# Performance work log

Hardware: AMD Instinct MI355X
Metric: run time of the kernel (lower is better)

The kernel has to match this reference:

```python
import jax, jax.numpy as jnp
import numpy as np

B, N1, N2, D, R = 4, 128, 128, 256, 4


def setup_inputs() -> dict:
    key = jax.random.key(0)
    ks = jax.random.split(key, 8)
    s = 0.02  # small init scale for weights
    return {
        "features1": jax.random.normal(ks[0], (B, N1, D), jnp.float32),
        "features2": jax.random.normal(ks[1], (B, N2, D), jnp.float32),
        # relation nets stacked over R: Linear(2D->D), Linear(D->D//2), Linear(D//2->1)
        "W1": jax.random.normal(ks[2], (R, 2 * D, D), jnp.float32) * s,
        "b1": jnp.zeros((R, D), jnp.float32),
        "W2": jax.random.normal(ks[3], (R, D, D // 2), jnp.float32) * s,
        "b2": jnp.zeros((R, D // 2), jnp.float32),
        "w3": jax.random.normal(ks[4], (R, D // 2), jnp.float32) * s,
        "b3": jnp.zeros((R,), jnp.float32),
        # aggregator: Linear(D*R -> 2D), Linear(2D -> D)
        "Wa1": jax.random.normal(ks[5], (D * R, 2 * D), jnp.float32) * s,
        "ba1": jnp.zeros((2 * D,), jnp.float32),
        "Wa2": jax.random.normal(ks[6], (2 * D, D), jnp.float32) * s,
        "ba2": jnp.zeros((D,), jnp.float32),
    }


def reference(features1, features2, W1, b1, W2, b2, w3, b3, Wa1, ba1, Wa2, ba2):
    b, n1, d = features1.shape
    n2 = features2.shape[1]
    r = W1.shape[0]
    # concat([f1_i, f2_j]) @ W1 == f1_i @ W1[:d] + f2_j @ W1[d:]
    W1a, W1b = W1[:, :d, :], W1[:, d:, :]
    h1 = jnp.einsum('bid,rde->brie', features1, W1a)          # [B,R,N1,D]
    h2 = jnp.einsum('bjd,rde->brje', features2, W1b)          # [B,R,N2,D]
    h = jax.nn.relu(h1[:, :, :, None, :] + h2[:, :, None, :, :]
                    + b1[None, :, None, None, :])             # [B,R,N1,N2,D]
    g = jax.nn.relu(jnp.einsum('brijd,rde->brije', h, W2)
                    + b2[None, :, None, None, :])             # [B,R,N1,N2,D//2]
    scores = jnp.einsum('brije,re->brij', g, w3) + b3[None, :, None, None]
    w = jax.nn.softmax(scores, axis=-1)                       # softmax over j (N2)
    rel = jnp.einsum('brij,bjd->brid', w, features2)          # [B,R,N1,D]
    # torch cat over relations along feature dim -> relation index outermost
    all_rel = rel.transpose(0, 2, 1, 3).reshape(b, n1, r * d)  # [B,N1,R*D]
    out = jax.nn.relu(all_rel @ Wa1 + ba1) @ Wa2 + ba2         # [B,N1,D]
    return out
```

## Files before the change

kernel.cpp:

```cpp
#include <hip/hip_runtime.h>


typedef _Float16 f16x8 __attribute__((ext_vector_type(8)));
typedef float f32x16 __attribute__((ext_vector_type(16)));

static __device__ __forceinline__ ushort to_h(float f) {
  _Float16 h = (_Float16)f;
  return __builtin_bit_cast(ushort, h);
}
static __device__ __forceinline__ uint pack2(float a, float b) {
  return (uint)to_h(a) | ((uint)to_h(b) << 16);
}
static __device__ __forceinline__ uint pk_add(uint a, uint b) {
  uint r;
  asm("v_pk_add_f16 %0, %1, %2" : "=v"(r) : "v"(a), "v"(b));
  return r;
}
static __device__ __forceinline__ uint pk_relu(uint a) {
  uint r;
  asm("v_pk_max_f16 %0, %1, %2" : "=v"(r) : "v"(a), "v"(0u));
  return r;
}

__global__ __launch_bounds__(256) void k_prep(
    const float* __restrict__ f1, const float* __restrict__ f2,
    const float* __restrict__ W1, const float* __restrict__ W2,
    const float* __restrict__ Wa1, const float* __restrict__ Wa2,
    uint* __restrict__ f1hp, uint* __restrict__ f2hp,
    ushort* __restrict__ W1swz, ushort* __restrict__ W2swz,
    ushort* __restrict__ f2swz, ushort* __restrict__ Wa1swz,
    ushort* __restrict__ Wa2swz)
{
  int blk = blockIdx.x, t = threadIdx.x;
  if (blk < 128) {
    int u = blk * 256 + t;
    float4 a = *(const float4*)&f1[u * 4];
    float4 b = *(const float4*)&f2[u * 4];
    *(uint2*)&f1hp[u * 2] = make_uint2(pack2(a.x, a.y), pack2(a.z, a.w));
    *(uint2*)&f2hp[u * 2] = make_uint2(pack2(b.x, b.y), pack2(b.z, b.w));
    return;
  }
  if (blk < 256) {
    int unit = blk - 128;
    int r = unit >> 5, half = (unit >> 4) & 1, ks = unit & 15;
    int l = t & 63, ctq = t >> 6;
    #pragma unroll
    for (int ci = 0; ci < 2; ++ci) {
      int ct = ctq + ci * 4;
      int e = ct * 32 + (l & 31);
      ushort us[8];
      #pragma unroll
      for (int j = 0; j < 8; ++j) {
        int d = ks * 16 + ((l >> 5) * 4) + (j & 3) + ((j >> 2) * 8);
        us[j] = to_h(W1[(size_t)(r * 512 + half * 256 + d) * 256 + e]);
      }
      uint4 pk;
      pk.x = (uint)us[0] | ((uint)us[1] << 16);
      pk.y = (uint)us[2] | ((uint)us[3] << 16);
      pk.z = (uint)us[4] | ((uint)us[5] << 16);
      pk.w = (uint)us[6] | ((uint)us[7] << 16);
      *(uint4*)&W1swz[(size_t)((((r * 2 + half) * 16 + ks) * 8 + ct) * 64 + l) * 8] = pk;
    }
    return;
  }
  if (blk < 272) {
    int sub = blk - 256;
    int r = sub >> 2, ks0 = (sub & 3) * 4;
    int ct = t >> 6, l = t & 63;
    #pragma unroll
    for (int ko = 0; ko < 4; ++ko) {
      int ks = ks0 + ko;
      ushort us[8];
      #pragma unroll
      for (int j = 0; j < 8; ++j) {
        int d = ks * 16 + ((j >> 2) * 8) + ((l >> 5) * 4) + (j & 3);
        int e = ct * 32 + (l & 31);
        us[j] = to_h(W2[(r * 256 + d) * 128 + e]);
      }
      uint4 pk;
      pk.x = (uint)us[0] | ((uint)us[1] << 16);
      pk.y = (uint)us[2] | ((uint)us[3] << 16);
      pk.z = (uint)us[4] | ((uint)us[5] << 16);
      pk.w = (uint)us[6] | ((uint)us[7] << 16);
      *(uint4*)&W2swz[(((r * 16 + ks) * 4 + ct) * 64 + l) * 8] = pk;
    }
    return;
  }
  if (blk < 288) {
    int sub = blk - 272;
    int w = t >> 6, l = t & 63;
    #pragma unroll
    for (int ko = 0; ko < 4; ++ko) {
      int u = sub * 16 + w * 4 + ko;
      int b = u >> 6, ks = (u >> 3) & 7, ctg = u & 7;
      ushort us[8];
      #pragma unroll
      for (int j = 0; j < 8; ++j) {
        int k = ks * 16 + ((l >> 5) * 4) + (j & 3) + ((j >> 2) * 8);
        int n = ctg * 32 + (l & 31);
        us[j] = to_h(f2[((size_t)b * 128 + k) * 256 + n]);
      }
      uint4 pk;
      pk.x = (uint)us[0] | ((uint)us[1] << 16);
      pk.y = (uint)us[2] | ((uint)us[3] << 16);
      pk.z = (uint)us[4] | ((uint)us[5] << 16);
      pk.w = (uint)us[6] | ((uint)us[7] << 16);
      *(uint4*)&f2swz[(((b * 8 + ks) * 8 + ctg) * 64 + l) * 8] = pk;
    }
    return;
  }
  if (blk < 304) {
    int sub = blk - 288;
    #pragma unroll
    for (int ko = 0; ko < 16; ++ko) {
      int id = sub * 4096 + ko * 256 + t;
      int ks = id >> 10, ct = (id >> 6) & 15, l = id & 63;
      ushort us[8];
      #pragma unroll
      for (int j = 0; j < 8; ++j) {
        int d = ks * 16 + ((l >> 5) * 4) + (j & 3) + ((j >> 2) * 8);
        int e = ct * 32 + (l & 31);
        us[j] = to_h(Wa1[(size_t)d * 512 + e]);
      }
      uint4 pk;
      pk.x = (uint)us[0] | ((uint)us[1] << 16);
      pk.y = (uint)us[2] | ((uint)us[3] << 16);
      pk.z = (uint)us[4] | ((uint)us[5] << 16);
      pk.w = (uint)us[6] | ((uint)us[7] << 16);
      *(uint4*)&Wa1swz[(size_t)id * 8] = pk;
    }
    return;
  }
  {
    int sub = blk - 304;
    #pragma unroll
    for (int ko = 0; ko < 4; ++ko) {
      int id = sub * 1024 + ko * 256 + t;
      int ks = id >> 9, ct = (id >> 6) & 7, l = id & 63;
      ushort us[8];
      #pragma unroll
      for (int j = 0; j < 8; ++j) {
        int d = ks * 16 + ((l >> 5) * 4) + (j & 3) + ((j >> 2) * 8);
        int e = ct * 32 + (l & 31);
        us[j] = to_h(Wa2[(size_t)d * 256 + e]);
      }
      uint4 pk;
      pk.x = (uint)us[0] | ((uint)us[1] << 16);
      pk.y = (uint)us[2] | ((uint)us[3] << 16);
      pk.z = (uint)us[4] | ((uint)us[5] << 16);
      pk.w = (uint)us[6] | ((uint)us[7] << 16);
      *(uint4*)&Wa2swz[(size_t)id * 8] = pk;
    }
    return;
  }
}

__global__ __launch_bounds__(256) void k_proj_mfma(
    const uint* __restrict__ f1hp, const uint* __restrict__ f2hp,
    const ushort* __restrict__ W1swz, const float* __restrict__ b1,
    ushort* __restrict__ h1p, ushort* __restrict__ h2)
{
  int bid = blockIdx.x;
  int it = bid & 3;
  int half = (bid >> 2) & 1;
  int r = (bid >> 3) & 3;
  int b = bid >> 5;
  int t = threadIdx.x, w = t >> 6, l = t & 63;
  __shared__ uint Au[32][132];

  const uint* src = (half ? f2hp : f1hp) + (size_t)b * 16384 + it * 32 * 128;
  #pragma unroll
  for (int q = 0; q < 4; ++q) {
    int lin = q * 256 + t;
    int row = lin >> 5, c4 = (lin & 31) * 4;
    *(uint4*)&Au[row][c4] = *(const uint4*)&src[row * 128 + c4];
  }
  __syncthreads();

  int m31 = l & 31, hi = l >> 5, hi2 = hi * 2;
  f32x16 acc0, acc1;
  #pragma unroll
  for (int e = 0; e < 16; ++e) { acc0[e] = 0.f; acc1[e] = 0.f; }

  const ushort* bb = W1swz + (size_t)(r * 2 + half) * 65536;
  for (int ks = 0; ks < 16; ++ks) {
    int u0 = ks * 8 + hi2;
    uint2 xa = *(const uint2*)&Au[m31][u0];
    uint2 xb = *(const uint2*)&Au[m31][u0 + 4];
    uint4 a4 = make_uint4(xa.x, xa.y, xb.x, xb.y);
    f16x8 af = __builtin_bit_cast(f16x8, a4);
    uint4 br0 = *(const uint4*)&bb[((ks * 8 + w * 2 + 0) * 64 + l) * 8];
    uint4 br1 = *(const uint4*)&bb[((ks * 8 + w * 2 + 1) * 64 + l) * 8];
    f16x8 bf0 = __builtin_bit_cast(f16x8, br0);
    f16x8 bf1 = __builtin_bit_cast(f16x8, br1);
    acc0 = __builtin_amdgcn_mfma_f32_32x32x16_f16(af, bf0, acc0, 0, 0, 0);
    acc1 = __builtin_amdgcn_mfma_f32_32x32x16_f16(af, bf1, acc1, 0, 0, 0);
  }

  ushort* ho = (half ? h2 : h1p) + ((size_t)((b * 4 + r) * 128 + it * 32)) * 256;
  #pragma unroll
  for (int ctl = 0; ctl < 2; ++ctl) {
    int e = (w * 2 + ctl) * 32 + m31;
    float bv = half ? 0.f : b1[r * 256 + e];
    #pragma unroll
    for (int g = 0; g < 16; ++g) {
      int row = (g & 3) + 8 * (g >> 2) + 4 * hi;
      ho[row * 256 + e] = to_h((ctl ? acc1[g] : acc0[g]) + bv);
    }
  }
}

__global__ __launch_bounds__(256, 4) void k_scores_mfma(
    const ushort* __restrict__ h1p, const ushort* __restrict__ h2,
    const ushort* __restrict__ W2swz, const float* __restrict__ b2,
    const float* __restrict__ w3, const float* __restrict__ b3,
    float* __restrict__ scores)
{
  int bid = blockIdx.x;
  int jt = bid & 7;
  int it = (bid >> 3) & 15;
  int r  = (bid >> 7) & 3;
  int b  = bid >> 9;
  int t = threadIdx.x, w = t >> 6, l = t & 63;
  __shared__ uint h1u[8][132];
  __shared__ uint h2u[16][132];
  __shared__ float xch[4][2][2][16];

  const uint* h1g = (const uint*)h1p + ((size_t)((b * 4 + r) * 128 + it * 8)) * 128;
  const uint* h2g = (const uint*)h2  + ((size_t)((b * 4 + r) * 128 + jt * 16)) * 128;
  {
    int row = t >> 5, c4 = (t & 31) * 4;
    *(uint4*)&h1u[row][c4] = *(const uint4*)&h1g[row * 128 + c4];
    *(uint4*)&h2u[row][c4] = *(const uint4*)&h2g[row * 128 + c4];
    *(uint4*)&h2u[row + 8][c4] = *(const uint4*)&h2g[(row + 8) * 128 + c4];
  }

  f32x16 acc[2][2];
  #pragma unroll
  for (int i = 0; i < 2; ++i)
    #pragma unroll
    for (int c = 0; c < 2; ++c)
      #pragma unroll
      for (int e = 0; e < 16; ++e) acc[i][c][e] = 0.f;

  int rtp = w & 1, ctp = w >> 1;
  int hi2 = (l >> 5) * 2;
  int m31 = l & 31;
  int jrow = m31 & 15;
  int irow0 = (rtp * 2 + 0) * 2 + (m31 >> 4);
  int irow1 = (rtp * 2 + 1) * 2 + (m31 >> 4);
  const ushort* bptr = W2swz + r * (16 * 4 * 64 * 8);

  __syncthreads();

  const uint* h1r0 = &h1u[irow0][0];
  const uint* h1r1 = &h1u[irow1][0];
  const uint* h2r  = &h2u[jrow][0];
  for (int ks = 0; ks < 16; ++ks) {
    int u0 = ks * 8 + hi2;
    uint2 ya  = *(const uint2*)&h2r[u0];
    uint2 yb  = *(const uint2*)&h2r[u0 + 4];
    uint2 xa0 = *(const uint2*)&h1r0[u0];
    uint2 xb0 = *(const uint2*)&h1r0[u0 + 4];
    uint2 xa1 = *(const uint2*)&h1r1[u0];
    uint2 xb1 = *(const uint2*)&h1r1[u0 + 4];
    uint4 pk0, pk1;
    pk0.x = pk_relu(pk_add(xa0.x, ya.x));
    pk0.y = pk_relu(pk_add(xa0.y, ya.y));
    pk0.z = pk_relu(pk_add(xb0.x, yb.x));
    pk0.w = pk_relu(pk_add(xb0.y, yb.y));
    pk1.x = pk_relu(pk_add(xa1.x, ya.x));
    pk1.y = pk_relu(pk_add(xa1.y, ya.y));
    pk1.z = pk_relu(pk_add(xb1.x, yb.x));
    pk1.w = pk_relu(pk_add(xb1.y, yb.y));
    f16x8 af0 = __builtin_bit_cast(f16x8, pk0);
    f16x8 af1 = __builtin_bit_cast(f16x8, pk1);
    uint4 braw0 = *(const uint4*)&bptr[((ks * 4 + ctp * 2 + 0) * 64 + l) * 8];
    uint4 braw1 = *(const uint4*)&bptr[((ks * 4 + ctp * 2 + 1) * 64 + l) * 8];
    f16x8 bf0 = __builtin_bit_cast(f16x8, braw0);
    f16x8 bf1 = __builtin_bit_cast(f16x8, braw1);
    acc[0][0] = __builtin_amdgcn_mfma_f32_32x32x16_f16(af0, bf0, acc[0][0], 0, 0, 0);
    acc[0][1] = __builtin_amdgcn_mfma_f32_32x32x16_f16(af0, bf1, acc[0][1], 0, 0, 0);
    acc[1][0] = __builtin_amdgcn_mfma_f32_32x32x16_f16(af1, bf0, acc[1][0], 0, 0, 0);
    acc[1][1] = __builtin_amdgcn_mfma_f32_32x32x16_f16(af1, bf1, acc[1][1], 0, 0, 0);
  }

  float sp[2][16];
  #pragma unroll
  for (int i = 0; i < 2; ++i)
    #pragma unroll
    for (int g = 0; g < 16; ++g) sp[i][g] = 0.f;
  #pragma unroll
  for (int ctl = 0; ctl < 2; ++ctl) {
    int e = (ctp * 2 + ctl) * 32 + m31;
    float w3v = w3[r * 128 + e];
    float b2v = b2[r * 128 + e];
    #pragma unroll
    for (int i = 0; i < 2; ++i)
      #pragma unroll
      for (int g = 0; g < 16; ++g)
        sp[i][g] = fmaf(w3v, fmaxf(acc[i][ctl][g] + b2v, 0.f), sp[i][g]);
  }
  #pragma unroll
  for (int off = 16; off >= 1; off >>= 1)
    #pragma unroll
    for (int i = 0; i < 2; ++i)
      #pragma unroll
      for (int g = 0; g < 16; ++g)
        sp[i][g] += __shfl_xor(sp[i][g], off, 64);
  int hi = l >> 5;
  if (m31 == 0) {
    #pragma unroll
    for (int i = 0; i < 2; ++i)
      #pragma unroll
      for (int g = 0; g < 16; ++g)
        xch[w][i][hi][g] = sp[i][g];
  }
  __syncthreads();
  if (w < 2 && m31 == 0) {
    float b3v = b3[r];
    float* sc_base = scores + (((b * 4 + r) * 128 + it * 8) * 128) + jt * 16;
    #pragma unroll
    for (int i = 0; i < 2; ++i)
      #pragma unroll
      for (int g = 0; g < 16; ++g) {
        float s = xch[w][i][hi][g] + xch[w + 2][i][hi][g] + b3v;
        int p = (w * 2 + i) * 32 + (g & 3) + 8 * (g >> 2) + hi * 4;
        sc_base[(p >> 4) * 128 + (p & 15)] = s;
      }
  }
}

__global__ __launch_bounds__(64, 1) void k_softrel_mfma(
    const float* __restrict__ scores, const ushort* __restrict__ f2swz,
    ushort* __restrict__ all_rel_h)
{
  int bid = blockIdx.x;
  int rowq = bid & 3;
  int nh = (bid >> 2) & 1;
  int r  = (bid >> 3) & 3;
  int b  = bid >> 5;
  int l = threadIdx.x;
  int row = rowq * 32 + (l & 31);
  const float* srow = scores + ((size_t)(b * 4 + r) * 128 + row) * 128;

  float p[128];
  #pragma unroll
  for (int q = 0; q < 32; ++q) {
    float4 v = *(const float4*)&srow[q * 4];
    p[q * 4 + 0] = v.x; p[q * 4 + 1] = v.y;
    p[q * 4 + 2] = v.z; p[q * 4 + 3] = v.w;
  }
  float m = p[0];
  #pragma unroll
  for (int j = 1; j < 128; ++j) m = fmaxf(m, p[j]);
  float sum = 0.f;
  #pragma unroll
  for (int j = 0; j < 128; ++j) { p[j] = __expf(p[j] - m); sum += p[j]; }
  float inv = 1.f / sum;
  uint preg[64];
  #pragma unroll
  for (int q = 0; q < 64; ++q)
    preg[q] = pack2(p[2 * q] * inv, p[2 * q + 1] * inv);

  f32x16 acc[4];
  #pragma unroll
  for (int c = 0; c < 4; ++c)
    #pragma unroll
    for (int e = 0; e < 16; ++e) acc[c][e] = 0.f;

  int hi2 = (l >> 5) * 2;
  const ushort* bbase = f2swz + (size_t)b * (8 * 8 * 64 * 8);
  #pragma unroll
  for (int ks = 0; ks < 8; ++ks) {
    int b2i = ks * 8 + hi2;
    uint4 pk = make_uint4(preg[b2i], preg[b2i + 1], preg[b2i + 4], preg[b2i + 5]);
    f16x8 af = __builtin_bit_cast(f16x8, pk);
    #pragma unroll
    for (int ct = 0; ct < 4; ++ct) {
      uint4 braw = *(const uint4*)&bbase[((ks * 8 + nh * 4 + ct) * 64 + l) * 8];
      f16x8 bfr = __builtin_bit_cast(f16x8, braw);
      acc[ct] = __builtin_amdgcn_mfma_f32_32x32x16_f16(af, bfr, acc[ct], 0, 0, 0);
    }
  }

  ushort* dst = all_rel_h + (size_t)(b * 128) * 1024;
  int ebase = r * 256 + nh * 128 + (l & 31);
  int half4 = (l >> 5) << 2;
  #pragma unroll
  for (int ct = 0; ct < 4; ++ct)
    #pragma unroll
    for (int g = 0; g < 16; ++g) {
      int i = rowq * 32 + (g & 3) + 8 * (g >> 2) + half4;
      dst[(size_t)i * 1024 + ebase + ct * 32] = to_h(acc[ct][g]);
    }
}

__global__ __launch_bounds__(256) void k_mlp1(
    const ushort* __restrict__ all_rel_h, const ushort* __restrict__ Wa1swz,
    const float* __restrict__ ba1, ushort* __restrict__ hiddenh)
{
  int cq = blockIdx.x, rt = blockIdx.y;
  int t = threadIdx.x, w = t >> 6, l = t & 63;
  __shared__ uint Ah[32][514];
  const uint* Ag = (const uint*)all_rel_h + (size_t)rt * 32 * 512;
  #pragma unroll
  for (int q = 0; q < 16; ++q) {
    int lin = q * 256 + t;
    int row = lin >> 7, c4 = (lin & 127) * 4;
    *(uint4*)&Ah[row][c4] = *(const uint4*)&Ag[row * 512 + c4];
  }
  __syncthreads();

  int m31 = l & 31, hi = l >> 5, hi2 = hi * 2;
  int ct = cq * 4 + w;
  f32x16 acc;
  #pragma unroll
  for (int e = 0; e < 16; ++e) acc[e] = 0.f;
  for (int ks = 0; ks < 64; ++ks) {
    int u0 = ks * 8 + hi2;
    uint2 xa = *(const uint2*)&Ah[m31][u0];
    uint2 xb = *(const uint2*)&Ah[m31][u0 + 4];
    uint4 a4 = make_uint4(xa.x, xa.y, xb.x, xb.y);
    f16x8 af = __builtin_bit_cast(f16x8, a4);
    uint4 braw = *(const uint4*)&Wa1swz[(size_t)((ks * 16 + ct) * 64 + l) * 8];
    f16x8 bfr = __builtin_bit_cast(f16x8, braw);
    acc = __builtin_amdgcn_mfma_f32_32x32x16_f16(af, bfr, acc, 0, 0, 0);
  }
  int e = ct * 32 + m31;
  float bv = ba1[e];
  #pragma unroll
  for (int g = 0; g < 16; ++g) {
    int row = (g & 3) + 8 * (g >> 2) + 4 * hi;
    hiddenh[(size_t)(rt * 32 + row) * 512 + e] = to_h(fmaxf(acc[g] + bv, 0.f));
  }
}

__global__ __launch_bounds__(256) void k_mlp2(
    const ushort* __restrict__ hiddenh, const ushort* __restrict__ Wa2swz,
    const float* __restrict__ ba2, float* __restrict__ out)
{
  int cq = blockIdx.x, rt = blockIdx.y;
  int t = threadIdx.x, w = t >> 6, l = t & 63;
  __shared__ uint Ah[32][258];
  const uint* Ag = (const uint*)hiddenh + (size_t)rt * 32 * 256;
  #pragma unroll
  for (int q = 0; q < 8; ++q) {
    int lin = q * 256 + t;
    int row = lin >> 6, c4 = (lin & 63) * 4;
    *(uint4*)&Ah[row][c4] = *(const uint4*)&Ag[row * 256 + c4];
  }
  __syncthreads();

  int m31 = l & 31, hi = l >> 5, hi2 = hi * 2;
  int ct = cq * 4 + w;
  f32x16 acc;
  #pragma unroll
  for (int e = 0; e < 16; ++e) acc[e] = 0.f;
  for (int ks = 0; ks < 32; ++ks) {
    int u0 = ks * 8 + hi2;
    uint2 xa = *(const uint2*)&Ah[m31][u0];
    uint2 xb = *(const uint2*)&Ah[m31][u0 + 4];
    uint4 a4 = make_uint4(xa.x, xa.y, xb.x, xb.y);
    f16x8 af = __builtin_bit_cast(f16x8, a4);
    uint4 braw = *(const uint4*)&Wa2swz[(size_t)((ks * 8 + ct) * 64 + l) * 8];
    f16x8 bfr = __builtin_bit_cast(f16x8, braw);
    acc = __builtin_amdgcn_mfma_f32_32x32x16_f16(af, bfr, acc, 0, 0, 0);
  }
  int e = ct * 32 + m31;
  float bv = ba2[e];
  #pragma unroll
  for (int g = 0; g < 16; ++g) {
    int row = (g & 3) + 8 * (g >> 2) + 4 * hi;
    out[(size_t)(rt * 32 + row) * 256 + e] = acc[g] + bv;
  }
}

extern "C" void kernel_launch(void* const* d_in, const int* in_sizes, int n_in,
                              void* d_out, int out_size, void* d_ws, size_t ws_size,
                              hipStream_t stream) {
  const float* f1  = (const float*)d_in[0];
  const float* f2  = (const float*)d_in[1];
  const float* W1  = (const float*)d_in[2];
  const float* b1  = (const float*)d_in[3];
  const float* W2  = (const float*)d_in[4];
  const float* b2  = (const float*)d_in[5];
  const float* w3  = (const float*)d_in[6];
  const float* b3  = (const float*)d_in[7];
  const float* Wa1 = (const float*)d_in[8];
  const float* ba1 = (const float*)d_in[9];
  const float* Wa2 = (const float*)d_in[10];
  const float* ba2 = (const float*)d_in[11];
  float* out = (float*)d_out;
  float* ws = (float*)d_ws;

  uint*   f1hp     = (uint*)ws;
  uint*   f2hp     = (uint*)(ws + 65536);
  ushort* h1p      = (ushort*)(ws + 131072);
  ushort* h2       = (ushort*)(ws + 393216);
  float*  scores   = ws + 655360;
  ushort* all_relh = (ushort*)(ws + 917504);
  ushort* W1swz    = (ushort*)(ws + 1179648);
  ushort* W2swz    = (ushort*)(ws + 1441792);
  ushort* f2swz    = (ushort*)(ws + 1507328);
  ushort* Wa1swz   = (ushort*)(ws + 1572864);
  ushort* Wa2swz   = (ushort*)(ws + 1835008);
  ushort* hiddenh  = (ushort*)(ws + 1900544);

  hipLaunchKernelGGL(k_prep, dim3(320), dim3(256), 0, stream,
                     f1, f2, W1, W2, Wa1, Wa2,
                     f1hp, f2hp, W1swz, W2swz, f2swz, Wa1swz, Wa2swz);
  hipLaunchKernelGGL(k_proj_mfma, dim3(128), dim3(256), 0, stream,
                     f1hp, f2hp, W1swz, b1, h1p, h2);
  hipLaunchKernelGGL(k_scores_mfma, dim3(2048), dim3(256), 0, stream,
                     h1p, h2, W2swz, b2, w3, b3, scores);
  hipLaunchKernelGGL(k_softrel_mfma, dim3(128), dim3(64), 0, stream,
                     scores, f2swz, all_relh);
  hipLaunchKernelGGL(k_mlp1, dim3(4, 16), dim3(256), 0, stream,
                     all_relh, Wa1swz, ba1, hiddenh);
  hipLaunchKernelGGL(k_mlp2, dim3(2, 16), dim3(256), 0, stream,
                     hiddenh, Wa2swz, ba2, out);
}
```

Before: 64.58 us.

## Prefetch W2 fragments in scores loop and split softrel work across more blocks

```diff
diff --git a/kernel.cpp b/kernel.cpp
--- a/kernel.cpp
+++ b/kernel.cpp
@@ -249,14 +249,22 @@
   int jrow = m31 & 15;
   int irow0 = (rtp * 2 + 0) * 2 + (m31 >> 4);
   int irow1 = (rtp * 2 + 1) * 2 + (m31 >> 4);
-  const ushort* bptr = W2swz + r * (16 * 4 * 64 * 8);
+  const ushort* bptr = W2swz + r * (16 * 4 * 64 * 8) + (((ctp * 2) * 64 + l) * 8);
 
   __syncthreads();
 
   const uint* h1r0 = &h1u[irow0][0];
   const uint* h1r1 = &h1u[irow1][0];
   const uint* h2r  = &h2u[jrow][0];
+  uint4 nb0 = *(const uint4*)&bptr[0];
+  uint4 nb1 = *(const uint4*)&bptr[512];
+  #pragma unroll 2
   for (int ks = 0; ks < 16; ++ks) {
+    uint4 b0 = nb0, b1 = nb1;
+    if (ks < 15) {
+      nb0 = *(const uint4*)&bptr[(ks + 1) * 2048];
+      nb1 = *(const uint4*)&bptr[(ks + 1) * 2048 + 512];
+    }
     int u0 = ks * 8 + hi2;
     uint2 ya  = *(const uint2*)&h2r[u0];
     uint2 yb  = *(const uint2*)&h2r[u0 + 4];
@@ -275,10 +283,8 @@
     pk1.w = pk_relu(pk_add(xb1.y, yb.y));
     f16x8 af0 = __builtin_bit_cast(f16x8, pk0);
     f16x8 af1 = __builtin_bit_cast(f16x8, pk1);
-    uint4 braw0 = *(const uint4*)&bptr[((ks * 4 + ctp * 2 + 0) * 64 + l) * 8];
-    uint4 braw1 = *(const uint4*)&bptr[((ks * 4 + ctp * 2 + 1) * 64 + l) * 8];
-    f16x8 bf0 = __builtin_bit_cast(f16x8, braw0);
-    f16x8 bf1 = __builtin_bit_cast(f16x8, braw1);
+    f16x8 bf0 = __builtin_bit_cast(f16x8, b0);
+    f16x8 bf1 = __builtin_bit_cast(f16x8, b1);
     acc[0][0] = __builtin_amdgcn_mfma_f32_32x32x16_f16(af0, bf0, acc[0][0], 0, 0, 0);
     acc[0][1] = __builtin_amdgcn_mfma_f32_32x32x16_f16(af0, bf1, acc[0][1], 0, 0, 0);
     acc[1][0] = __builtin_amdgcn_mfma_f32_32x32x16_f16(af1, bf0, acc[1][0], 0, 0, 0);
@@ -336,10 +342,11 @@
     ushort* __restrict__ all_rel_h)
 {
   int bid = blockIdx.x;
-  int rowq = bid & 3;
-  int nh = (bid >> 2) & 1;
-  int r  = (bid >> 3) & 3;
-  int b  = bid >> 5;
+  int ctp  = bid & 1;
+  int rowq = (bid >> 1) & 3;
+  int nh   = (bid >> 3) & 1;
+  int r    = (bid >> 4) & 3;
+  int b    = bid >> 6;
   int l = threadIdx.x;
   int row = rowq * 32 + (l & 31);
   const float* srow = scores + ((size_t)(b * 4 + r) * 128 + row) * 128;
@@ -351,21 +358,35 @@
     p[q * 4 + 0] = v.x; p[q * 4 + 1] = v.y;
     p[q * 4 + 2] = v.z; p[q * 4 + 3] = v.w;
   }
-  float m = p[0];
-  #pragma unroll
-  for (int j = 1; j < 128; ++j) m = fmaxf(m, p[j]);
-  float sum = 0.f;
-  #pragma unroll
-  for (int j = 0; j < 128; ++j) { p[j] = __expf(p[j] - m); sum += p[j]; }
+  float mm[8];
+  #pragma unroll
+  for (int c = 0; c < 8; ++c) mm[c] = p[c * 16];
+  #pragma unroll
+  for (int k = 1; k < 16; ++k)
+    #pragma unroll
+    for (int c = 0; c < 8; ++c) mm[c] = fmaxf(mm[c], p[c * 16 + k]);
+  float m = fmaxf(fmaxf(fmaxf(mm[0], mm[1]), fmaxf(mm[2], mm[3])),
+                  fmaxf(fmaxf(mm[4], mm[5]), fmaxf(mm[6], mm[7])));
+  float ss[8];
+  #pragma unroll
+  for (int c = 0; c < 8; ++c) ss[c] = 0.f;
+  #pragma unroll
+  for (int k = 0; k < 16; ++k)
+    #pragma unroll
+    for (int c = 0; c < 8; ++c) {
+      p[c * 16 + k] = __expf(p[c * 16 + k] - m);
+      ss[c] += p[c * 16 + k];
+    }
+  float sum = ((ss[0] + ss[1]) + (ss[2] + ss[3])) + ((ss[4] + ss[5]) + (ss[6] + ss[7]));
   float inv = 1.f / sum;
   uint preg[64];
   #pragma unroll
   for (int q = 0; q < 64; ++q)
     preg[q] = pack2(p[2 * q] * inv, p[2 * q + 1] * inv);
 
-  f32x16 acc[4];
-  #pragma unroll
-  for (int c = 0; c < 4; ++c)
+  f32x16 acc[2];
+  #pragma unroll
+  for (int c = 0; c < 2; ++c)
     #pragma unroll
     for (int e = 0; e < 16; ++e) acc[c][e] = 0.f;
 
@@ -377,22 +398,23 @@
     uint4 pk = make_uint4(preg[b2i], preg[b2i + 1], preg[b2i + 4], preg[b2i + 5]);
     f16x8 af = __builtin_bit_cast(f16x8, pk);
     #pragma unroll
-    for (int ct = 0; ct < 4; ++ct) {
-      uint4 braw = *(const uint4*)&bbase[((ks * 8 + nh * 4 + ct) * 64 + l) * 8];
+    for (int ctl = 0; ctl < 2; ++ctl) {
+      int ct = nh * 4 + ctp * 2 + ctl;
+      uint4 braw = *(const uint4*)&bbase[((ks * 8 + ct) * 64 + l) * 8];
       f16x8 bfr = __builtin_bit_cast(f16x8, braw);
-      acc[ct] = __builtin_amdgcn_mfma_f32_32x32x16_f16(af, bfr, acc[ct], 0, 0, 0);
+      acc[ctl] = __builtin_amdgcn_mfma_f32_32x32x16_f16(af, bfr, acc[ctl], 0, 0, 0);
     }
   }
 
   ushort* dst = all_rel_h + (size_t)(b * 128) * 1024;
-  int ebase = r * 256 + nh * 128 + (l & 31);
+  int ebase = r * 256 + nh * 128 + ctp * 64 + (l & 31);
   int half4 = (l >> 5) << 2;
   #pragma unroll
-  for (int ct = 0; ct < 4; ++ct)
+  for (int ctl = 0; ctl < 2; ++ctl)
     #pragma unroll
     for (int g = 0; g < 16; ++g) {
       int i = rowq * 32 + (g & 3) + 8 * (g >> 2) + half4;
-      dst[(size_t)i * 1024 + ebase + ct * 32] = to_h(acc[ct][g]);
+      dst[(size_t)i * 1024 + ebase + ctl * 32] = to_h(acc[ctl][g]);
     }
 }
 
@@ -514,7 +536,7 @@
                      f1hp, f2hp, W1swz, b1, h1p, h2);
   hipLaunchKernelGGL(k_scores_mfma, dim3(2048), dim3(256), 0, stream,
                      h1p, h2, W2swz, b2, w3, b3, scores);
-  hipLaunchKernelGGL(k_softrel_mfma, dim3(128), dim3(64), 0, stream,
+  hipLaunchKernelGGL(k_softrel_mfma, dim3(256), dim3(64), 0, stream,
                      scores, f2swz, all_relh);
   hipLaunchKernelGGL(k_mlp1, dim3(4, 16), dim3(256), 0, stream,
                      all_relh, Wa1swz, ba1, hiddenh);
```

Result: faster. 62.35 us (-3.5%).
